# Kernel optimization log

Measured on AMD Instinct MI355X. Metric: run time of the kernel, lower is better.

## Reference

```python
import jax, jax.numpy as jnp
import numpy as np

D = 1024

def setup_inputs() -> dict:
    key = jax.random.key(0)
    ks = jax.random.split(key, 7)
    s = 1.0 / np.sqrt(D)
    return {
        "x": jax.random.normal(ks[0], (4, 2048, D), dtype=jnp.float32),
        "Wq": jax.random.uniform(ks[1], (D, D), jnp.float32, -s, s),
        "bq": jax.random.uniform(ks[2], (D,), jnp.float32, -s, s),
        "Wk": jax.random.uniform(ks[3], (D, D), jnp.float32, -s, s),
        "bk": jax.random.uniform(ks[4], (D,), jnp.float32, -s, s),
        "Wv": jax.random.uniform(ks[5], (D, D), jnp.float32, -s, s),
        "bv": jax.random.uniform(ks[6], (D,), jnp.float32, -s, s),
    }

def reference(x, Wq, bq, Wk, bk, Wv, bv):
    # x: [b, s, d]; Linear layers: y = x @ W^T + b (torch convention)
    q = jnp.einsum('bsd,ed->bse', x, Wq) + bq
    k = jnp.einsum('bsd,ed->bse', x, Wk) + bk
    v = jnp.einsum('bsd,ed->bse', x, Wv) + bv
    # NOTE: original module does NOT scale by 1/sqrt(d)
    scores = jnp.einsum('bqd,bkd->bqk', q, k)  # [b, s, s]
    attn = jax.nn.softmax(scores, axis=-1)
    return jnp.einsum('bqk,bkd->bqd', attn, v)
```

## Files before the change

kernel.cpp:

```cpp
#include <hip/hip_runtime.h>

typedef _Float16 half8 __attribute__((ext_vector_type(8)));
typedef float floatx4 __attribute__((ext_vector_type(4)));

__device__ __forceinline__ void gld_lds16(const void* g, void* l) {
  __builtin_amdgcn_global_load_lds(
      (const __attribute__((address_space(1))) void*)g,
      (__attribute__((address_space(3))) void*)l, 16, 0, 0);
}

#define SB() __builtin_amdgcn_sched_barrier(0)
#define LGKM(n) asm volatile("s_waitcnt lgkmcnt(" #n ")" ::: "memory")
#define VMC(n) asm volatile("s_waitcnt vmcnt(" #n ")" ::: "memory")
#define PRIO1() __builtin_amdgcn_s_setprio(1)
#define PRIO0() __builtin_amdgcn_s_setprio(0)

template <int MODE>
__global__ __launch_bounds__(512, 2) void gemm4(
    const _Float16* __restrict__ Ag, const _Float16* __restrict__ Bg,
    void* __restrict__ Cg, const float* __restrict__ bcat) {
  constexpr int TN   = MODE == 0 ? 192 : (MODE == 1 ? 256 : 128);
  constexpr int STR  = MODE == 0 ? 1024 : (MODE == 1 ? 3072 : 2048);
  constexpr int NK   = (MODE == 2 ? 2048 : 1024) / 64;
  constexpr int NWG  = MODE == 0 ? 512 : 256;
  constexpr int NBC  = TN / 64;
  constexpr int BBUF = TN * 64;
  constexpr int CSTR = MODE == 0 ? 3072 : (MODE == 1 ? 2048 : 1024);

  int g = (int)blockIdx.x;
  g = (g & 7) * (NWG / 8) + (g >> 3);

  int row0, col0;
  const _Float16 *Ap, *Bp;
  _Float16* C16 = nullptr;
  float* C32 = nullptr;
  if constexpr (MODE == 0) {
    const int tm = g >> 4, tn = g & 15;
    row0 = tm * 256; col0 = tn * 192;
    Ap = Ag + (size_t)row0 * 1024;
    Bp = Bg + (size_t)col0 * 1024;
    C16 = (_Float16*)Cg;
  } else if constexpr (MODE == 1) {
    const int z = g >> 6, r = g & 63, tm = r >> 3, tn = r & 7;
    row0 = tm * 256; col0 = tn * 256;
    Ap = Ag + (size_t)z * 6291456 + (size_t)row0 * 3072;
    Bp = Ag + (size_t)z * 6291456 + (size_t)col0 * 3072 + 1024;
    C16 = (_Float16*)Cg + (size_t)z * 4194304;
  } else {
    const int z = g >> 6, r = g & 63, tm = r >> 3, tn = r & 7;
    row0 = tm * 256; col0 = tn * 128;
    Ap = Ag + (size_t)z * 4194304 + (size_t)row0 * 2048;
    Bp = Bg + (size_t)z * 2097152 + (size_t)col0 * 2048;
    C32 = (float*)Cg + (size_t)z * 2097152;
  }

  __shared__ _Float16 lds[32768 + 2 * BBUF];
  const int tid = threadIdx.x, lane = tid & 63, wid = tid >> 6;
  const int wave_m = MODE == 2 ? (wid >> 1) : (wid >> 2);
  const int wave_n = MODE == 2 ? (wid & 1) : (wid & 3);
  const int fr = lane & 15, u = lane >> 4, w7 = lane & 7;
  const int k0e = ((u ^ w7) << 3), k1e = (((4 + u) ^ w7) << 3);
  const int sgl = (((tid & 7) ^ ((tid >> 3) & 7)) << 3);
  const int srow = tid >> 3;

  floatx4 acc[MODE == 2 ? 4 : 8][MODE == 0 ? 3 : 4] = {};
  half8 aF0[8], aF1[8], bF0[4], bF1[4];

  auto stage1 = [&](const _Float16* Gp, int r0c, int kt, int dst) {
    gld_lds16(Gp + (size_t)(r0c + srow) * STR + kt + sgl, &lds[dst + tid * 8]);
  };
  auto ldAq = [&](int bufA, int qm, half8* dst) {
    const int rb = MODE == 2 ? wave_m * 64 : (wave_m * 128 + qm * 64);
#pragma unroll
    for (int mf = 0; mf < 4; ++mf) {
      const int ro = bufA + (rb + mf * 16 + fr) * 64;
      dst[mf * 2 + 0] = *(const half8*)&lds[ro + k0e];
      dst[mf * 2 + 1] = *(const half8*)&lds[ro + k1e];
    }
  };
  auto ldB2 = [&](int bufB, int qh, half8* dst) {
    const int cb = (MODE == 0 ? wave_n * 48 : wave_n * 64) + qh * 32;
#pragma unroll
    for (int nf = 0; nf < 2; ++nf) {
      const int ro = bufB + (cb + nf * 16 + fr) * 64;
      dst[nf * 2 + 0] = *(const half8*)&lds[ro + k0e];
      dst[nf * 2 + 1] = *(const half8*)&lds[ro + k1e];
    }
  };
  auto ldB1 = [&](int bufB, half8* dst) {
    const int ro = bufB + (wave_n * 48 + 32 + fr) * 64;
    dst[0] = *(const half8*)&lds[ro + k0e];
    dst[1] = *(const half8*)&lds[ro + k1e];
  };
  auto QUADx2 = [&](int am0, half8* aF, int nb, half8* bF) {
#pragma unroll
    for (int mf = 0; mf < 4; ++mf)
#pragma unroll
      for (int nf = 0; nf < 2; ++nf)
#pragma unroll
        for (int kk = 0; kk < 2; ++kk)
          acc[am0 + mf][nb + nf] = __builtin_amdgcn_mfma_f32_16x16x32_f16(
              aF[mf * 2 + kk], bF[nf * 2 + kk], acc[am0 + mf][nb + nf], 0, 0, 0);
  };
  auto QUADx1 = [&](int am0, half8* aF, half8* bF) {
#pragma unroll
    for (int mf = 0; mf < 4; ++mf)
#pragma unroll
      for (int kk = 0; kk < 2; ++kk)
        acc[am0 + mf][2] = __builtin_amdgcn_mfma_f32_16x16x32_f16(
            aF[mf * 2 + kk], bF[kk], acc[am0 + mf][2], 0, 0, 0);
  };

#pragma unroll
  for (int c = 0; c < 4; ++c) stage1(Ap, c * 64, 0, c * 4096);
#pragma unroll
  for (int c = 0; c < NBC; ++c) stage1(Bp, c * 64, 0, 32768 + c * 4096);
#pragma unroll
  for (int c = 0; c < NBC; ++c) stage1(Bp, c * 64, 64, 32768 + BBUF + c * 4096);
  if constexpr (NBC == 4) VMC(4); else if constexpr (NBC == 3) VMC(3); else VMC(2);
  __builtin_amdgcn_s_barrier();

#pragma unroll 1
  for (int t = 0; t < NK; ++t) {
    const int kt = t * 64;
    const int bufA = (t & 1) * 16384, obufA = ((t + 1) & 1) * 16384;
    const int bufB = 32768 + (t & 1) * BBUF;
    ldAq(bufA, 0, aF0); SB();
    ldB2(bufB, 0, bF0); SB();
    if constexpr (MODE == 0) { ldB1(bufB, bF1); } else { ldB2(bufB, 1, bF1); }
    SB();
    if constexpr (MODE != 2) { ldAq(bufA, 1, aF1); SB(); }
    if (t + 1 < NK) {
#pragma unroll
      for (int c = 0; c < 4; ++c) stage1(Ap, c * 64, kt + 64, obufA + c * 4096);
    }
    SB();
    if constexpr (MODE == 2) {
      LGKM(4); SB(); PRIO1(); QUADx2(0, aF0, 0, bF0); PRIO0(); SB();
      LGKM(0); SB();
      __builtin_amdgcn_s_barrier();
      if (t + 2 < NK) {
#pragma unroll
        for (int c = 0; c < 2; ++c) stage1(Bp, c * 64, kt + 128, bufB + c * 4096);
      }
      SB();
      PRIO1(); QUADx2(0, aF0, 2, bF1); PRIO0(); SB();
    } else if constexpr (MODE == 1) {
      LGKM(12); SB(); PRIO1(); QUADx2(0, aF0, 0, bF0); PRIO0(); SB();
      LGKM(8);  SB(); PRIO1(); QUADx2(0, aF0, 2, bF1); PRIO0(); SB();
      LGKM(0);  SB(); PRIO1(); QUADx2(4, aF1, 0, bF0); PRIO0(); SB();
      __builtin_amdgcn_s_barrier();
      if (t + 2 < NK) {
#pragma unroll
        for (int c = 0; c < 4; ++c) stage1(Bp, c * 64, kt + 128, bufB + c * 4096);
      }
      SB();
      PRIO1(); QUADx2(4, aF1, 2, bF1); PRIO0(); SB();
    } else {
      LGKM(10); SB(); PRIO1(); QUADx2(0, aF0, 0, bF0); PRIO0(); SB();
      LGKM(8);  SB(); PRIO1(); QUADx1(0, aF0, bF1); PRIO0(); SB();
      LGKM(0);  SB(); PRIO1(); QUADx2(4, aF1, 0, bF0); PRIO0(); SB();
      __builtin_amdgcn_s_barrier();
      if (t + 2 < NK) {
#pragma unroll
        for (int c = 0; c < 3; ++c) stage1(Bp, c * 64, kt + 128, bufB + c * 4096);
      }
      SB();
      PRIO1(); QUADx1(4, aF1, bF1); PRIO0(); SB();
    }
    if (t + 1 < NK) {
      if (t + 2 < NK) {
        if constexpr (NBC == 4) VMC(4); else if constexpr (NBC == 3) VMC(3); else VMC(2);
      } else VMC(0);
    }
    __builtin_amdgcn_s_barrier();
  }

  const int r0 = row0 + (MODE == 2 ? wave_m * 64 : wave_m * 128) + u * 4;
  const int c0 = col0 + (MODE == 0 ? wave_n * 48 : wave_n * 64) + fr;
  constexpr int NMT = MODE == 2 ? 4 : 8;
  constexpr int NFT = MODE == 0 ? 3 : 4;
#pragma unroll
  for (int m = 0; m < NMT; ++m)
#pragma unroll
    for (int n = 0; n < NFT; ++n) {
      const int col = c0 + n * 16;
      float badd = 0.f;
      if constexpr (MODE == 0) badd = bcat[col];
#pragma unroll
      for (int j = 0; j < 4; ++j) {
        const int row = r0 + m * 16 + j;
        if constexpr (MODE == 2)
          C32[(size_t)row * 1024 + col] = acc[m][n][j];
        else
          C16[(size_t)row * CSTR + col] = (_Float16)(acc[m][n][j] + badd);
      }
    }
}

__global__ void cvt_f32_f16(const float* __restrict__ in, _Float16* __restrict__ out, int n8) {
  int i = blockIdx.x * blockDim.x + threadIdx.x;
  const int stride = gridDim.x * blockDim.x;
  for (; i < n8; i += stride) {
    const float4* p = (const float4*)(in + (size_t)i * 8);
    float4 a = p[0], b = p[1];
    half8 h;
    h[0] = (_Float16)a.x; h[1] = (_Float16)a.y; h[2] = (_Float16)a.z; h[3] = (_Float16)a.w;
    h[4] = (_Float16)b.x; h[5] = (_Float16)b.y; h[6] = (_Float16)b.z; h[7] = (_Float16)b.w;
    *(half8*)(out + (size_t)i * 8) = h;
  }
}

__global__ void cvt3_w(const float* __restrict__ wq, const float* __restrict__ wk,
                       const float* __restrict__ wv, _Float16* __restrict__ out) {
  const float* in = blockIdx.y == 0 ? wq : (blockIdx.y == 1 ? wk : wv);
  _Float16* o = out + (size_t)blockIdx.y * 1048576;
  const int i = blockIdx.x * blockDim.x + threadIdx.x;
  const float4* p = (const float4*)(in + (size_t)i * 8);
  float4 a = p[0], b = p[1];
  half8 h;
  h[0] = (_Float16)a.x; h[1] = (_Float16)a.y; h[2] = (_Float16)a.z; h[3] = (_Float16)a.w;
  h[4] = (_Float16)b.x; h[5] = (_Float16)b.y; h[6] = (_Float16)b.z; h[7] = (_Float16)b.w;
  *(half8*)(o + (size_t)i * 8) = h;
}

__global__ void bias_cat(const float* __restrict__ a, const float* __restrict__ b,
                         const float* __restrict__ c, float* __restrict__ o) {
  const int i = blockIdx.x * 256 + threadIdx.x;
  const float* s = i < 1024 ? a : (i < 2048 ? b : c);
  o[i] = s[i & 1023];
}

__global__ __launch_bounds__(256) void transpose_v(const _Float16* __restrict__ QKV,
                                                   _Float16* __restrict__ Vt) {
  __shared__ _Float16 t[32][36];
  const int b = blockIdx.z;
  const int e0 = blockIdx.x * 32;
  const int s0 = blockIdx.y * 32;
  const int tid = threadIdx.x;
  const int r = tid >> 3;
  const int c4 = (tid & 7) * 4;
  const _Float16* src = QKV + (size_t)(b * 2048 + s0 + r) * 3072 + 2048 + e0 + c4;
#pragma unroll
  for (int j = 0; j < 4; ++j) t[r][c4 + j] = src[j];
  __syncthreads();
  _Float16* dst = Vt + ((size_t)b * 1024 + e0 + r) * 2048 + s0 + c4;
#pragma unroll
  for (int j = 0; j < 4; ++j) dst[j] = t[c4 + j][r];
}

__global__ __launch_bounds__(256) void softmax_rows_f16(_Float16* __restrict__ S) {
  __shared__ float red[4];
  _Float16* s = S + (size_t)blockIdx.x * 2048;
  const int tid = threadIdx.x;
  float v[8];
  {
    half8 h = *(const half8*)(s + tid * 8);
#pragma unroll
    for (int j = 0; j < 8; ++j) v[j] = (float)h[j];
  }
  float m = v[0];
#pragma unroll
  for (int j = 1; j < 8; ++j) m = fmaxf(m, v[j]);
#pragma unroll
  for (int off = 32; off > 0; off >>= 1) m = fmaxf(m, __shfl_xor(m, off));
  if ((tid & 63) == 0) red[tid >> 6] = m;
  __syncthreads();
  m = fmaxf(fmaxf(red[0], red[1]), fmaxf(red[2], red[3]));
  float sum = 0.f;
#pragma unroll
  for (int j = 0; j < 8; ++j) { v[j] = __expf(v[j] - m); sum += v[j]; }
#pragma unroll
  for (int off = 32; off > 0; off >>= 1) sum += __shfl_xor(sum, off);
  __syncthreads();
  if ((tid & 63) == 0) red[tid >> 6] = sum;
  __syncthreads();
  sum = red[0] + red[1] + red[2] + red[3];
  const float inv = 1.0f / sum;
  half8 h;
#pragma unroll
  for (int j = 0; j < 8; ++j) h[j] = (_Float16)(v[j] * inv);
  *(half8*)(s + tid * 8) = h;
}

extern "C" void kernel_launch(void* const* d_in, const int* in_sizes, int n_in,
                              void* d_out, int out_size, void* d_ws, size_t ws_size,
                              hipStream_t stream) {
  (void)in_sizes; (void)n_in; (void)out_size;
  const float* x  = (const float*)d_in[0];
  const float* Wq = (const float*)d_in[1];
  const float* bq = (const float*)d_in[2];
  const float* Wk = (const float*)d_in[3];
  const float* bk = (const float*)d_in[4];
  const float* Wv = (const float*)d_in[5];
  const float* bv = (const float*)d_in[6];
  float* out = (float*)d_out;

  char* ws = (char*)d_ws;
  size_t off = 0;
  auto alloc = [&](size_t bytes) {
    char* p = ws + off;
    off += (bytes + 255) & ~255ull;
    return p;
  };
  _Float16* x16  = (_Float16*)alloc(8192ull * 1024 * 2);
  _Float16* W16  = (_Float16*)alloc(3072ull * 1024 * 2);
  _Float16* QKV  = (_Float16*)alloc(8192ull * 3072 * 2);
  _Float16* Vt   = (_Float16*)alloc(4096ull * 1024 * 4);
  _Float16* Sc   = (_Float16*)alloc(4ull * 2048 * 2048 * 2);
  float*    bcat = (float*)alloc(3072 * 4);
  if (off > ws_size) return;

  cvt_f32_f16<<<2048, 256, 0, stream>>>(x, x16, 8192 * 1024 / 8);
  cvt3_w<<<dim3(512, 3), 256, 0, stream>>>(Wq, Wk, Wv, W16);
  bias_cat<<<12, 256, 0, stream>>>(bq, bk, bv, bcat);

  gemm4<0><<<512, 512, 0, stream>>>(x16, W16, QKV, bcat);
  transpose_v<<<dim3(32, 64, 4), 256, 0, stream>>>(QKV, Vt);

  gemm4<1><<<256, 512, 0, stream>>>(QKV, QKV, Sc, nullptr);
  softmax_rows_f16<<<8192, 256, 0, stream>>>(Sc);
  gemm4<2><<<256, 512, 0, stream>>>(Sc, Vt, out, nullptr);
}
```

Before: 165.3 us.

## Rewrite attention GEMMs with 32x32x16 MFMA and per-GEMM specialized kernels

Replaces the templated 16x16x32 MFMA GEMM with three dedicated kernels that use 32x32x16 MFMA instructions. The QKV projection moves to 128x384 tiles, and staging now loads full A+B tiles into double-buffered LDS with barrier-separated burst phases. Larger MFMA tiles cut LDS fragment reads per flop, at the cost of more barriers per iteration, changed overlap of global loads, and larger accumulator register pressure.

```diff
diff --git a/kernel.cpp b/kernel.cpp
--- a/kernel.cpp
+++ b/kernel.cpp
@@ -1,7 +1,7 @@
 #include <hip/hip_runtime.h>
 
 typedef _Float16 half8 __attribute__((ext_vector_type(8)));
-typedef float floatx4 __attribute__((ext_vector_type(4)));
+typedef float f32x16 __attribute__((ext_vector_type(16)));
 
 __device__ __forceinline__ void gld_lds16(const void* g, void* l) {
   __builtin_amdgcn_global_load_lds(
@@ -10,190 +10,264 @@
 }
 
 #define SB() __builtin_amdgcn_sched_barrier(0)
-#define LGKM(n) asm volatile("s_waitcnt lgkmcnt(" #n ")" ::: "memory")
+#define LGKM0() asm volatile("s_waitcnt lgkmcnt(0)" ::: "memory")
+#define LGKM8() asm volatile("s_waitcnt lgkmcnt(8)" ::: "memory")
 #define VMC(n) asm volatile("s_waitcnt vmcnt(" #n ")" ::: "memory")
+#define BAR() __builtin_amdgcn_s_barrier()
 #define PRIO1() __builtin_amdgcn_s_setprio(1)
 #define PRIO0() __builtin_amdgcn_s_setprio(0)
 
-template <int MODE>
-__global__ __launch_bounds__(512, 2) void gemm4(
-    const _Float16* __restrict__ Ag, const _Float16* __restrict__ Bg,
-    void* __restrict__ Cg, const float* __restrict__ bcat) {
-  constexpr int TN   = MODE == 0 ? 192 : (MODE == 1 ? 256 : 128);
-  constexpr int STR  = MODE == 0 ? 1024 : (MODE == 1 ? 3072 : 2048);
-  constexpr int NK   = (MODE == 2 ? 2048 : 1024) / 64;
-  constexpr int NWG  = MODE == 0 ? 512 : 256;
-  constexpr int NBC  = TN / 64;
-  constexpr int BBUF = TN * 64;
-  constexpr int CSTR = MODE == 0 ? 3072 : (MODE == 1 ? 2048 : 1024);
-
+
+__global__ __launch_bounds__(512, 2) void gemm32s(const _Float16* __restrict__ QKV,
+                                                  _Float16* __restrict__ Sc) {
   int g = (int)blockIdx.x;
-  g = (g & 7) * (NWG / 8) + (g >> 3);
-
-  int row0, col0;
-  const _Float16 *Ap, *Bp;
-  _Float16* C16 = nullptr;
-  float* C32 = nullptr;
-  if constexpr (MODE == 0) {
-    const int tm = g >> 4, tn = g & 15;
-    row0 = tm * 256; col0 = tn * 192;
-    Ap = Ag + (size_t)row0 * 1024;
-    Bp = Bg + (size_t)col0 * 1024;
-    C16 = (_Float16*)Cg;
-  } else if constexpr (MODE == 1) {
-    const int z = g >> 6, r = g & 63, tm = r >> 3, tn = r & 7;
-    row0 = tm * 256; col0 = tn * 256;
-    Ap = Ag + (size_t)z * 6291456 + (size_t)row0 * 3072;
-    Bp = Ag + (size_t)z * 6291456 + (size_t)col0 * 3072 + 1024;
-    C16 = (_Float16*)Cg + (size_t)z * 4194304;
-  } else {
-    const int z = g >> 6, r = g & 63, tm = r >> 3, tn = r & 7;
-    row0 = tm * 256; col0 = tn * 128;
-    Ap = Ag + (size_t)z * 4194304 + (size_t)row0 * 2048;
-    Bp = Bg + (size_t)z * 2097152 + (size_t)col0 * 2048;
-    C32 = (float*)Cg + (size_t)z * 2097152;
-  }
-
-  __shared__ _Float16 lds[32768 + 2 * BBUF];
+  g = (g & 7) * 32 + (g >> 3);
+  const int z = g >> 6, r = g & 63, tm = r >> 3, tn = r & 7;
+  const int row0 = tm * 256, col0 = tn * 256;
+  const _Float16* Ap = QKV + ((size_t)z * 2048 + row0) * 3072;
+  const _Float16* Bp = QKV + ((size_t)z * 2048 + col0) * 3072 + 1024;
+  _Float16* C16 = Sc + (size_t)z * 4194304;
+
+  __shared__ _Float16 lds[65536];
   const int tid = threadIdx.x, lane = tid & 63, wid = tid >> 6;
-  const int wave_m = MODE == 2 ? (wid >> 1) : (wid >> 2);
-  const int wave_n = MODE == 2 ? (wid & 1) : (wid & 3);
-  const int fr = lane & 15, u = lane >> 4, w7 = lane & 7;
-  const int k0e = ((u ^ w7) << 3), k1e = (((4 + u) ^ w7) << 3);
-  const int sgl = (((tid & 7) ^ ((tid >> 3) & 7)) << 3);
+  const int wm = wid >> 2, wn = wid & 3;
+  const int l31 = lane & 31, hi = lane >> 5, r7 = l31 & 7;
   const int srow = tid >> 3;
-
-  floatx4 acc[MODE == 2 ? 4 : 8][MODE == 0 ? 3 : 4] = {};
-  half8 aF0[8], aF1[8], bF0[4], bF1[4];
-
-  auto stage1 = [&](const _Float16* Gp, int r0c, int kt, int dst) {
-    gld_lds16(Gp + (size_t)(r0c + srow) * STR + kt + sgl, &lds[dst + tid * 8]);
-  };
-  auto ldAq = [&](int bufA, int qm, half8* dst) {
-    const int rb = MODE == 2 ? wave_m * 64 : (wave_m * 128 + qm * 64);
-#pragma unroll
-    for (int mf = 0; mf < 4; ++mf) {
-      const int ro = bufA + (rb + mf * 16 + fr) * 64;
-      dst[mf * 2 + 0] = *(const half8*)&lds[ro + k0e];
-      dst[mf * 2 + 1] = *(const half8*)&lds[ro + k1e];
-    }
-  };
-  auto ldB2 = [&](int bufB, int qh, half8* dst) {
-    const int cb = (MODE == 0 ? wave_n * 48 : wave_n * 64) + qh * 32;
-#pragma unroll
-    for (int nf = 0; nf < 2; ++nf) {
-      const int ro = bufB + (cb + nf * 16 + fr) * 64;
-      dst[nf * 2 + 0] = *(const half8*)&lds[ro + k0e];
-      dst[nf * 2 + 1] = *(const half8*)&lds[ro + k1e];
-    }
-  };
-  auto ldB1 = [&](int bufB, half8* dst) {
-    const int ro = bufB + (wave_n * 48 + 32 + fr) * 64;
-    dst[0] = *(const half8*)&lds[ro + k0e];
-    dst[1] = *(const half8*)&lds[ro + k1e];
-  };
-  auto QUADx2 = [&](int am0, half8* aF, int nb, half8* bF) {
-#pragma unroll
-    for (int mf = 0; mf < 4; ++mf)
-#pragma unroll
-      for (int nf = 0; nf < 2; ++nf)
-#pragma unroll
-        for (int kk = 0; kk < 2; ++kk)
-          acc[am0 + mf][nb + nf] = __builtin_amdgcn_mfma_f32_16x16x32_f16(
-              aF[mf * 2 + kk], bF[nf * 2 + kk], acc[am0 + mf][nb + nf], 0, 0, 0);
-  };
-  auto QUADx1 = [&](int am0, half8* aF, half8* bF) {
-#pragma unroll
-    for (int mf = 0; mf < 4; ++mf)
-#pragma unroll
-      for (int kk = 0; kk < 2; ++kk)
-        acc[am0 + mf][2] = __builtin_amdgcn_mfma_f32_16x16x32_f16(
-            aF[mf * 2 + kk], bF[kk], acc[am0 + mf][2], 0, 0, 0);
-  };
-
-#pragma unroll
-  for (int c = 0; c < 4; ++c) stage1(Ap, c * 64, 0, c * 4096);
-#pragma unroll
-  for (int c = 0; c < NBC; ++c) stage1(Bp, c * 64, 0, 32768 + c * 4096);
-#pragma unroll
-  for (int c = 0; c < NBC; ++c) stage1(Bp, c * 64, 64, 32768 + BBUF + c * 4096);
-  if constexpr (NBC == 4) VMC(4); else if constexpr (NBC == 3) VMC(3); else VMC(2);
-  __builtin_amdgcn_s_barrier();
-
+  const int sgl = (((tid & 7) ^ (srow & 7)) << 3);
+
+  f32x16 acc[4][2] = {};
+  half8 aF[8], bF0[4], bF1[4];
+
+  auto stage = [&](const _Float16* Gp, int rowoff, int kt, int dstbase) {
+    gld_lds16(Gp + (size_t)(rowoff + srow) * 3072 + kt + sgl, &lds[dstbase + tid * 8]);
+  };
+  auto stageT = [&](int kt, int par) {
+#pragma unroll
+    for (int h = 0; h < 4; ++h) stage(Ap, h * 64, kt, par * 32768 + h * 4096);
+#pragma unroll
+    for (int h = 0; h < 4; ++h) stage(Bp, h * 64, kt, par * 32768 + 16384 + h * 4096);
+  };
+  auto ldA = [&](int par, int qmh) {
+    const int base = par * 32768 + (wm * 128 + qmh * 64 + l31) * 64;
+#pragma unroll
+    for (int mb = 0; mb < 2; ++mb)
+#pragma unroll
+      for (int ks = 0; ks < 4; ++ks)
+        aF[mb * 4 + ks] = *(const half8*)&lds[base + mb * 2048 + (((ks * 2 + hi) ^ r7) << 3)];
+  };
+  auto ldB = [&](int par, int nb, half8* bF) {
+    const int base = par * 32768 + 16384 + (wn * 64 + nb * 32 + l31) * 64;
+#pragma unroll
+    for (int ks = 0; ks < 4; ++ks)
+      bF[ks] = *(const half8*)&lds[base + (((ks * 2 + hi) ^ r7) << 3)];
+  };
+  auto burst = [&](int qmh, int nb, const half8* bF) {
+#pragma unroll
+    for (int ks = 0; ks < 4; ++ks)
+#pragma unroll
+      for (int ml = 0; ml < 2; ++ml)
+        acc[qmh * 2 + ml][nb] = __builtin_amdgcn_mfma_f32_32x32x16_f16(
+            aF[ml * 4 + ks], bF[ks], acc[qmh * 2 + ml][nb], 0, 0, 0);
+  };
+
+  stageT(0, 0);
+  stageT(64, 1);
+  VMC(8); BAR();
+  constexpr int NK = 16;
 #pragma unroll 1
   for (int t = 0; t < NK; ++t) {
-    const int kt = t * 64;
-    const int bufA = (t & 1) * 16384, obufA = ((t + 1) & 1) * 16384;
-    const int bufB = 32768 + (t & 1) * BBUF;
-    ldAq(bufA, 0, aF0); SB();
-    ldB2(bufB, 0, bF0); SB();
-    if constexpr (MODE == 0) { ldB1(bufB, bF1); } else { ldB2(bufB, 1, bF1); }
-    SB();
-    if constexpr (MODE != 2) { ldAq(bufA, 1, aF1); SB(); }
-    if (t + 1 < NK) {
-#pragma unroll
-      for (int c = 0; c < 4; ++c) stage1(Ap, c * 64, kt + 64, obufA + c * 4096);
+    const int par = t & 1;
+    ldA(par, 0); SB(); ldB(par, 0, bF0); SB(); LGKM8();
+    BAR(); LGKM0(); SB(); PRIO1(); burst(0, 0, bF0); PRIO0(); SB(); BAR();
+    ldB(par, 1, bF1); SB();
+    BAR(); LGKM0(); SB(); PRIO1(); burst(0, 1, bF1); PRIO0(); SB(); BAR();
+    ldA(par, 1); SB();
+    BAR(); LGKM0(); SB(); PRIO1(); burst(1, 0, bF0); PRIO0(); SB(); BAR();
+    if (t + 2 < NK) stageT(t * 64 + 128, par);
+    SB(); PRIO1(); burst(1, 1, bF1); PRIO0(); SB();
+    if (t + 2 < NK) { VMC(8); } else if (t + 1 < NK) { VMC(0); }
+    BAR();
+  }
+
+  const int cb = col0 + wn * 64 + l31;
+#pragma unroll
+  for (int mb = 0; mb < 4; ++mb)
+#pragma unroll
+    for (int nb = 0; nb < 2; ++nb) {
+      const int col = cb + nb * 32;
+#pragma unroll
+      for (int j = 0; j < 16; ++j) {
+        const int row = row0 + wm * 128 + mb * 32 + (j & 3) + ((j >> 2) << 3) + hi * 4;
+        C16[(size_t)row * 2048 + col] = (_Float16)acc[mb][nb][j];
+      }
     }
-    SB();
-    if constexpr (MODE == 2) {
-      LGKM(4); SB(); PRIO1(); QUADx2(0, aF0, 0, bF0); PRIO0(); SB();
-      LGKM(0); SB();
-      __builtin_amdgcn_s_barrier();
-      if (t + 2 < NK) {
-#pragma unroll
-        for (int c = 0; c < 2; ++c) stage1(Bp, c * 64, kt + 128, bufB + c * 4096);
+}
+
+__global__ __launch_bounds__(512, 2) void gemm32q(const _Float16* __restrict__ Ag,
+                                                  const _Float16* __restrict__ Bg,
+                                                  _Float16* __restrict__ Cg,
+                                                  const float* __restrict__ bcat) {
+  int g = (int)blockIdx.x;
+  g = (g & 7) * 64 + (g >> 3);
+  const int tm = g >> 3, tn = g & 7;
+  const int row0 = tm * 128, col0 = tn * 384;
+  const _Float16* Ap = Ag + (size_t)row0 * 1024;
+  const _Float16* Bp = Bg + (size_t)col0 * 1024;
+
+  __shared__ _Float16 lds[65536];
+  const int tid = threadIdx.x, lane = tid & 63, wid = tid >> 6;
+  const int wm = wid >> 2, wn = wid & 3;
+  const int l31 = lane & 31, hi = lane >> 5, r7 = l31 & 7;
+  const int srow = tid >> 3;
+  const int sgl = (((tid & 7) ^ (srow & 7)) << 3);
+
+  f32x16 acc[2][3] = {};
+  half8 aF[8], bF[3][4];
+
+  auto stage = [&](const _Float16* Gp, int rowoff, int kt, int dstbase) {
+    gld_lds16(Gp + (size_t)(rowoff + srow) * 1024 + kt + sgl, &lds[dstbase + tid * 8]);
+  };
+  auto stageT = [&](int kt, int par) {
+#pragma unroll
+    for (int h = 0; h < 2; ++h) stage(Ap, h * 64, kt, par * 32768 + h * 4096);
+#pragma unroll
+    for (int h = 0; h < 6; ++h) stage(Bp, h * 64, kt, par * 32768 + 8192 + h * 4096);
+  };
+  auto ldA = [&](int par) {
+    const int base = par * 32768 + (wm * 64 + l31) * 64;
+#pragma unroll
+    for (int mb = 0; mb < 2; ++mb)
+#pragma unroll
+      for (int ks = 0; ks < 4; ++ks)
+        aF[mb * 4 + ks] = *(const half8*)&lds[base + mb * 2048 + (((ks * 2 + hi) ^ r7) << 3)];
+  };
+  auto ldB = [&](int par, int nb) {
+    const int base = par * 32768 + 8192 + (wn * 96 + nb * 32 + l31) * 64;
+#pragma unroll
+    for (int ks = 0; ks < 4; ++ks)
+      bF[nb][ks] = *(const half8*)&lds[base + (((ks * 2 + hi) ^ r7) << 3)];
+  };
+  auto burst = [&](int nb) {
+#pragma unroll
+    for (int ks = 0; ks < 4; ++ks)
+#pragma unroll
+      for (int mb = 0; mb < 2; ++mb)
+        acc[mb][nb] = __builtin_amdgcn_mfma_f32_32x32x16_f16(
+            aF[mb * 4 + ks], bF[nb][ks], acc[mb][nb], 0, 0, 0);
+  };
+
+  stageT(0, 0);
+  VMC(0); BAR();
+  constexpr int NK = 16;
+#pragma unroll 1
+  for (int t = 0; t < NK; ++t) {
+    const int par = t & 1;
+    ldA(par); SB(); ldB(par, 0); SB();
+    if (t + 1 < NK) stageT(t * 64 + 64, par ^ 1);
+    SB(); LGKM8();
+    BAR(); LGKM0(); SB(); PRIO1(); burst(0); PRIO0(); SB(); BAR();
+    ldB(par, 1); SB();
+    BAR(); LGKM0(); SB(); PRIO1(); burst(1); PRIO0(); SB(); BAR();
+    ldB(par, 2); SB();
+    BAR(); LGKM0(); SB(); PRIO1(); burst(2); PRIO0(); SB();
+    if (t + 1 < NK) VMC(0);
+    BAR();
+  }
+
+  const int cb = col0 + wn * 96 + l31;
+#pragma unroll
+  for (int mb = 0; mb < 2; ++mb)
+#pragma unroll
+    for (int nb = 0; nb < 3; ++nb) {
+      const int col = cb + nb * 32;
+      const float badd = bcat[col];
+#pragma unroll
+      for (int j = 0; j < 16; ++j) {
+        const int row = row0 + wm * 64 + mb * 32 + (j & 3) + ((j >> 2) << 3) + hi * 4;
+        Cg[(size_t)row * 3072 + col] = (_Float16)(acc[mb][nb][j] + badd);
       }
-      SB();
-      PRIO1(); QUADx2(0, aF0, 2, bF1); PRIO0(); SB();
-    } else if constexpr (MODE == 1) {
-      LGKM(12); SB(); PRIO1(); QUADx2(0, aF0, 0, bF0); PRIO0(); SB();
-      LGKM(8);  SB(); PRIO1(); QUADx2(0, aF0, 2, bF1); PRIO0(); SB();
-      LGKM(0);  SB(); PRIO1(); QUADx2(4, aF1, 0, bF0); PRIO0(); SB();
-      __builtin_amdgcn_s_barrier();
-      if (t + 2 < NK) {
-#pragma unroll
-        for (int c = 0; c < 4; ++c) stage1(Bp, c * 64, kt + 128, bufB + c * 4096);
-      }
-      SB();
-      PRIO1(); QUADx2(4, aF1, 2, bF1); PRIO0(); SB();
-    } else {
-      LGKM(10); SB(); PRIO1(); QUADx2(0, aF0, 0, bF0); PRIO0(); SB();
-      LGKM(8);  SB(); PRIO1(); QUADx1(0, aF0, bF1); PRIO0(); SB();
-      LGKM(0);  SB(); PRIO1(); QUADx2(4, aF1, 0, bF0); PRIO0(); SB();
-      __builtin_amdgcn_s_barrier();
-      if (t + 2 < NK) {
-#pragma unroll
-        for (int c = 0; c < 3; ++c) stage1(Bp, c * 64, kt + 128, bufB + c * 4096);
-      }
-      SB();
-      PRIO1(); QUADx1(4, aF1, bF1); PRIO0(); SB();
     }
-    if (t + 1 < NK) {
-      if (t + 2 < NK) {
-        if constexpr (NBC == 4) VMC(4); else if constexpr (NBC == 3) VMC(3); else VMC(2);
-      } else VMC(0);
-    }
-    __builtin_amdgcn_s_barrier();
-  }
-
-  const int r0 = row0 + (MODE == 2 ? wave_m * 64 : wave_m * 128) + u * 4;
-  const int c0 = col0 + (MODE == 0 ? wave_n * 48 : wave_n * 64) + fr;
-  constexpr int NMT = MODE == 2 ? 4 : 8;
-  constexpr int NFT = MODE == 0 ? 3 : 4;
-#pragma unroll
-  for (int m = 0; m < NMT; ++m)
-#pragma unroll
-    for (int n = 0; n < NFT; ++n) {
-      const int col = c0 + n * 16;
-      float badd = 0.f;
-      if constexpr (MODE == 0) badd = bcat[col];
-#pragma unroll
-      for (int j = 0; j < 4; ++j) {
-        const int row = r0 + m * 16 + j;
-        if constexpr (MODE == 2)
-          C32[(size_t)row * 1024 + col] = acc[m][n][j];
-        else
-          C16[(size_t)row * CSTR + col] = (_Float16)(acc[m][n][j] + badd);
+}
+
+__global__ __launch_bounds__(512, 2) void gemm32p(const _Float16* __restrict__ Scp,
+                                                  const _Float16* __restrict__ Vt,
+                                                  float* __restrict__ Out) {
+  int g = (int)blockIdx.x;
+  g = (g & 7) * 32 + (g >> 3);
+  const int z = g >> 6, r = g & 63, tm = r >> 3, tn = r & 7;
+  const int row0 = tm * 256, col0 = tn * 128;
+  const _Float16* Ap = Scp + (size_t)z * 4194304 + (size_t)row0 * 2048;
+  const _Float16* Bp = Vt + (size_t)z * 2097152 + (size_t)col0 * 2048;
+  float* C32 = Out + (size_t)z * 2097152;
+
+  __shared__ _Float16 lds[49152];
+  const int tid = threadIdx.x, lane = tid & 63, wid = tid >> 6;
+  const int wm = wid >> 1, wn = wid & 1;
+  const int l31 = lane & 31, hi = lane >> 5, r7 = l31 & 7;
+  const int srow = tid >> 3;
+  const int sgl = (((tid & 7) ^ (srow & 7)) << 3);
+
+  f32x16 acc[2][2] = {};
+  half8 aF[8], bF0[4], bF1[4];
+
+  auto stage = [&](const _Float16* Gp, int rowoff, int kt, int dstbase) {
+    gld_lds16(Gp + (size_t)(rowoff + srow) * 2048 + kt + sgl, &lds[dstbase + tid * 8]);
+  };
+  auto stageT = [&](int kt, int par) {
+#pragma unroll
+    for (int h = 0; h < 4; ++h) stage(Ap, h * 64, kt, par * 24576 + h * 4096);
+#pragma unroll
+    for (int h = 0; h < 2; ++h) stage(Bp, h * 64, kt, par * 24576 + 16384 + h * 4096);
+  };
+  auto ldA = [&](int par) {
+    const int base = par * 24576 + (wm * 64 + l31) * 64;
+#pragma unroll
+    for (int mb = 0; mb < 2; ++mb)
+#pragma unroll
+      for (int ks = 0; ks < 4; ++ks)
+        aF[mb * 4 + ks] = *(const half8*)&lds[base + mb * 2048 + (((ks * 2 + hi) ^ r7) << 3)];
+  };
+  auto ldB = [&](int par, int nb, half8* bF) {
+    const int base = par * 24576 + 16384 + (wn * 64 + nb * 32 + l31) * 64;
+#pragma unroll
+    for (int ks = 0; ks < 4; ++ks)
+      bF[ks] = *(const half8*)&lds[base + (((ks * 2 + hi) ^ r7) << 3)];
+  };
+  auto burst = [&](int nb, const half8* bF) {
+#pragma unroll
+    for (int ks = 0; ks < 4; ++ks)
+#pragma unroll
+      for (int mb = 0; mb < 2; ++mb)
+        acc[mb][nb] = __builtin_amdgcn_mfma_f32_32x32x16_f16(
+            aF[mb * 4 + ks], bF[ks], acc[mb][nb], 0, 0, 0);
+  };
+
+  stageT(0, 0);
+  VMC(0); BAR();
+  constexpr int NK = 32;
+#pragma unroll 1
+  for (int t = 0; t < NK; ++t) {
+    const int par = t & 1;
+    ldA(par); SB(); ldB(par, 0, bF0); SB();
+    if (t + 1 < NK) stageT(t * 64 + 64, par ^ 1);
+    SB(); LGKM8();
+    BAR(); LGKM0(); SB(); PRIO1(); burst(0, bF0); PRIO0(); SB(); BAR();
+    ldB(par, 1, bF1); SB();
+    BAR(); LGKM0(); SB(); PRIO1(); burst(1, bF1); PRIO0(); SB();
+    if (t + 1 < NK) VMC(0);
+    BAR();
+  }
+
+  const int cb = col0 + wn * 64 + l31;
+#pragma unroll
+  for (int mb = 0; mb < 2; ++mb)
+#pragma unroll
+    for (int nb = 0; nb < 2; ++nb) {
+      const int col = cb + nb * 32;
+#pragma unroll
+      for (int j = 0; j < 16; ++j) {
+        const int row = row0 + wm * 64 + mb * 32 + (j & 3) + ((j >> 2) << 3) + hi * 4;
+        C32[(size_t)row * 1024 + col] = acc[mb][nb][j];
       }
     }
 }
@@ -315,10 +389,10 @@
   cvt3_w<<<dim3(512, 3), 256, 0, stream>>>(Wq, Wk, Wv, W16);
   bias_cat<<<12, 256, 0, stream>>>(bq, bk, bv, bcat);
 
-  gemm4<0><<<512, 512, 0, stream>>>(x16, W16, QKV, bcat);
+  gemm32q<<<512, 512, 0, stream>>>(x16, W16, QKV, bcat);
   transpose_v<<<dim3(32, 64, 4), 256, 0, stream>>>(QKV, Vt);
 
-  gemm4<1><<<256, 512, 0, stream>>>(QKV, QKV, Sc, nullptr);
+  gemm32s<<<256, 512, 0, stream>>>(QKV, Sc);
   softmax_rows_f16<<<8192, 256, 0, stream>>>(Sc);
-  gemm4<2><<<256, 512, 0, stream>>>(Sc, Vt, out, nullptr);
-}
+  gemm32p<<<256, 512, 0, stream>>>(Sc, Vt, out);
+}
```

Measured after the change: 183.9 us. +11.3%, slower.

## Simplify GEMM pipeline to uniform double-buffered A/B staging with new wave layouts

Applied to the files above, without the earlier changes.

Replaces the staggered pipeline, where B was prefetched two steps ahead and A one step ahead with a mid-iteration barrier, with a plain double buffer. A and B for the next K step are issued together at the top of each iteration, followed by a single vmcnt(0) wait and one barrier per iteration. It also changes the wave tiling for the QKV and PV GEMMs from a 2x4 and 4x2 layout to 4x2 waves with 4 M fragments each. The aim is fewer barriers and simpler scheduling. The cost is that global loads have only one iteration of compute to hide behind, and a full vmcnt(0) drain every step.

```diff
diff --git a/kernel.cpp b/kernel.cpp
--- a/kernel.cpp
+++ b/kernel.cpp
@@ -11,20 +11,25 @@
 
 #define SB() __builtin_amdgcn_sched_barrier(0)
 #define LGKM(n) asm volatile("s_waitcnt lgkmcnt(" #n ")" ::: "memory")
-#define VMC(n) asm volatile("s_waitcnt vmcnt(" #n ")" ::: "memory")
+#define VMC0() asm volatile("s_waitcnt vmcnt(0)" ::: "memory")
+#define BAR() __builtin_amdgcn_s_barrier()
 #define PRIO1() __builtin_amdgcn_s_setprio(1)
 #define PRIO0() __builtin_amdgcn_s_setprio(0)
 
 template <int MODE>
-__global__ __launch_bounds__(512, 2) void gemm4(
+__global__ __launch_bounds__(512, 2) void gemmr(
     const _Float16* __restrict__ Ag, const _Float16* __restrict__ Bg,
     void* __restrict__ Cg, const float* __restrict__ bcat) {
   constexpr int TN   = MODE == 0 ? 192 : (MODE == 1 ? 256 : 128);
-  constexpr int STR  = MODE == 0 ? 1024 : (MODE == 1 ? 3072 : 2048);
-  constexpr int NK   = (MODE == 2 ? 2048 : 1024) / 64;
+  constexpr int KS   = MODE == 0 ? 1024 : (MODE == 1 ? 3072 : 2048);
+  constexpr int NK   = MODE == 2 ? 32 : 16;
   constexpr int NWG  = MODE == 0 ? 512 : 256;
-  constexpr int NBC  = TN / 64;
-  constexpr int BBUF = TN * 64;
+  constexpr int WN   = MODE == 1 ? 4 : 2;
+  constexpr int NMF  = MODE == 1 ? 8 : 4;
+  constexpr int NNF  = TN / 16 / WN;
+  constexpr int ASL  = 16384;
+  constexpr int BSL  = TN * 64;
+  constexpr int NSB  = TN / 64;
   constexpr int CSTR = MODE == 0 ? 3072 : (MODE == 1 ? 2048 : 1024);
 
   int g = (int)blockIdx.x;
@@ -54,146 +59,102 @@
     C32 = (float*)Cg + (size_t)z * 2097152;
   }
 
-  __shared__ _Float16 lds[32768 + 2 * BBUF];
+  __shared__ _Float16 lds[2 * ASL + 2 * BSL];
   const int tid = threadIdx.x, lane = tid & 63, wid = tid >> 6;
-  const int wave_m = MODE == 2 ? (wid >> 1) : (wid >> 2);
-  const int wave_n = MODE == 2 ? (wid & 1) : (wid & 3);
+  const int wm = MODE == 1 ? (wid >> 2) : (wid >> 1);
+  const int wn = MODE == 1 ? (wid & 3) : (wid & 1);
+  const int wrow = wm * (NMF * 16);
+  const int wcol = wn * (NNF * 16);
   const int fr = lane & 15, u = lane >> 4, w7 = lane & 7;
   const int k0e = ((u ^ w7) << 3), k1e = (((4 + u) ^ w7) << 3);
-  const int sgl = (((tid & 7) ^ ((tid >> 3) & 7)) << 3);
   const int srow = tid >> 3;
-
-  floatx4 acc[MODE == 2 ? 4 : 8][MODE == 0 ? 3 : 4] = {};
-  half8 aF0[8], aF1[8], bF0[4], bF1[4];
-
-  auto stage1 = [&](const _Float16* Gp, int r0c, int kt, int dst) {
-    gld_lds16(Gp + (size_t)(r0c + srow) * STR + kt + sgl, &lds[dst + tid * 8]);
-  };
-  auto ldAq = [&](int bufA, int qm, half8* dst) {
-    const int rb = MODE == 2 ? wave_m * 64 : (wave_m * 128 + qm * 64);
+  const int sgl = (((tid & 7) ^ (srow & 7)) << 3);
+
+  floatx4 acc[NMF][NNF] = {};
+  half8 aF[NMF * 2], bF[NNF * 2];
+
+  auto stage1 = [&](const _Float16* Gp, int rowoff, int kt, int dst) {
+    gld_lds16(Gp + (size_t)(rowoff + srow) * KS + kt + sgl, &lds[dst + tid * 8]);
+  };
+  auto stageT = [&](int kt, int p) {
+#pragma unroll
+    for (int c = 0; c < 4; ++c) stage1(Ap, c * 64, kt, p * ASL + c * 4096);
+#pragma unroll
+    for (int c = 0; c < NSB; ++c)
+      stage1(Bp, c * 64, kt, 2 * ASL + p * BSL + c * 4096);
+  };
+  auto ldA4 = [&](int p, int mf0) {
 #pragma unroll
     for (int mf = 0; mf < 4; ++mf) {
-      const int ro = bufA + (rb + mf * 16 + fr) * 64;
-      dst[mf * 2 + 0] = *(const half8*)&lds[ro + k0e];
-      dst[mf * 2 + 1] = *(const half8*)&lds[ro + k1e];
-    }
-  };
-  auto ldB2 = [&](int bufB, int qh, half8* dst) {
-    const int cb = (MODE == 0 ? wave_n * 48 : wave_n * 64) + qh * 32;
+      const int ro = p * ASL + (wrow + (mf0 + mf) * 16 + fr) * 64;
+      aF[(mf0 + mf) * 2 + 0] = *(const half8*)&lds[ro + k0e];
+      aF[(mf0 + mf) * 2 + 1] = *(const half8*)&lds[ro + k1e];
+    }
+  };
+  auto ldB2 = [&](int p, int nf0) {
 #pragma unroll
     for (int nf = 0; nf < 2; ++nf) {
-      const int ro = bufB + (cb + nf * 16 + fr) * 64;
-      dst[nf * 2 + 0] = *(const half8*)&lds[ro + k0e];
-      dst[nf * 2 + 1] = *(const half8*)&lds[ro + k1e];
-    }
-  };
-  auto ldB1 = [&](int bufB, half8* dst) {
-    const int ro = bufB + (wave_n * 48 + 32 + fr) * 64;
-    dst[0] = *(const half8*)&lds[ro + k0e];
-    dst[1] = *(const half8*)&lds[ro + k1e];
-  };
-  auto QUADx2 = [&](int am0, half8* aF, int nb, half8* bF) {
+      const int ro = 2 * ASL + p * BSL + (wcol + (nf0 + nf) * 16 + fr) * 64;
+      bF[(nf0 + nf) * 2 + 0] = *(const half8*)&lds[ro + k0e];
+      bF[(nf0 + nf) * 2 + 1] = *(const half8*)&lds[ro + k1e];
+    }
+  };
+  auto burst = [&](int mf0, int nf0) {
 #pragma unroll
     for (int mf = 0; mf < 4; ++mf)
 #pragma unroll
       for (int nf = 0; nf < 2; ++nf)
 #pragma unroll
         for (int kk = 0; kk < 2; ++kk)
-          acc[am0 + mf][nb + nf] = __builtin_amdgcn_mfma_f32_16x16x32_f16(
-              aF[mf * 2 + kk], bF[nf * 2 + kk], acc[am0 + mf][nb + nf], 0, 0, 0);
-  };
-  auto QUADx1 = [&](int am0, half8* aF, half8* bF) {
-#pragma unroll
-    for (int mf = 0; mf < 4; ++mf)
-#pragma unroll
-      for (int kk = 0; kk < 2; ++kk)
-        acc[am0 + mf][2] = __builtin_amdgcn_mfma_f32_16x16x32_f16(
-            aF[mf * 2 + kk], bF[kk], acc[am0 + mf][2], 0, 0, 0);
-  };
-
-#pragma unroll
-  for (int c = 0; c < 4; ++c) stage1(Ap, c * 64, 0, c * 4096);
-#pragma unroll
-  for (int c = 0; c < NBC; ++c) stage1(Bp, c * 64, 0, 32768 + c * 4096);
-#pragma unroll
-  for (int c = 0; c < NBC; ++c) stage1(Bp, c * 64, 64, 32768 + BBUF + c * 4096);
-  if constexpr (NBC == 4) VMC(4); else if constexpr (NBC == 3) VMC(3); else VMC(2);
-  __builtin_amdgcn_s_barrier();
+          acc[mf0 + mf][nf0 + nf] = __builtin_amdgcn_mfma_f32_16x16x32_f16(
+              aF[(mf0 + mf) * 2 + kk], bF[(nf0 + nf) * 2 + kk],
+              acc[mf0 + mf][nf0 + nf], 0, 0, 0);
+  };
+
+  stageT(0, 0);
+  VMC0();
+  BAR();
 
 #pragma unroll 1
   for (int t = 0; t < NK; ++t) {
-    const int kt = t * 64;
-    const int bufA = (t & 1) * 16384, obufA = ((t + 1) & 1) * 16384;
-    const int bufB = 32768 + (t & 1) * BBUF;
-    ldAq(bufA, 0, aF0); SB();
-    ldB2(bufB, 0, bF0); SB();
-    if constexpr (MODE == 0) { ldB1(bufB, bF1); } else { ldB2(bufB, 1, bF1); }
+    const int p = t & 1;
+    if (t + 1 < NK) stageT(t * 64 + 64, p ^ 1);
     SB();
-    if constexpr (MODE != 2) { ldAq(bufA, 1, aF1); SB(); }
-    if (t + 1 < NK) {
-#pragma unroll
-      for (int c = 0; c < 4; ++c) stage1(Ap, c * 64, kt + 64, obufA + c * 4096);
-    }
-    SB();
-    if constexpr (MODE == 2) {
-      LGKM(4); SB(); PRIO1(); QUADx2(0, aF0, 0, bF0); PRIO0(); SB();
-      LGKM(0); SB();
-      __builtin_amdgcn_s_barrier();
-      if (t + 2 < NK) {
-#pragma unroll
-        for (int c = 0; c < 2; ++c) stage1(Bp, c * 64, kt + 128, bufB + c * 4096);
-      }
-      SB();
-      PRIO1(); QUADx2(0, aF0, 2, bF1); PRIO0(); SB();
-    } else if constexpr (MODE == 1) {
-      LGKM(12); SB(); PRIO1(); QUADx2(0, aF0, 0, bF0); PRIO0(); SB();
-      LGKM(8);  SB(); PRIO1(); QUADx2(0, aF0, 2, bF1); PRIO0(); SB();
-      LGKM(0);  SB(); PRIO1(); QUADx2(4, aF1, 0, bF0); PRIO0(); SB();
-      __builtin_amdgcn_s_barrier();
-      if (t + 2 < NK) {
-#pragma unroll
-        for (int c = 0; c < 4; ++c) stage1(Bp, c * 64, kt + 128, bufB + c * 4096);
-      }
-      SB();
-      PRIO1(); QUADx2(4, aF1, 2, bF1); PRIO0(); SB();
+    if constexpr (MODE == 1) {
+      ldA4(p, 0); SB(); ldB2(p, 0); SB(); ldB2(p, 2); SB(); ldA4(p, 4); SB();
+      LGKM(12); SB(); PRIO1(); burst(0, 0); PRIO0(); SB();
+      LGKM(8);  SB(); PRIO1(); burst(0, 2); PRIO0(); SB();
+      LGKM(0);  SB(); PRIO1(); burst(4, 0); burst(4, 2); PRIO0(); SB();
+    } else if constexpr (MODE == 0) {
+      ldA4(p, 0); SB(); ldB2(p, 0); SB(); ldB2(p, 2); SB(); ldB2(p, 4); SB();
+      LGKM(8); SB(); PRIO1(); burst(0, 0); PRIO0(); SB();
+      LGKM(4); SB(); PRIO1(); burst(0, 2); PRIO0(); SB();
+      LGKM(0); SB(); PRIO1(); burst(0, 4); PRIO0(); SB();
     } else {
-      LGKM(10); SB(); PRIO1(); QUADx2(0, aF0, 0, bF0); PRIO0(); SB();
-      LGKM(8);  SB(); PRIO1(); QUADx1(0, aF0, bF1); PRIO0(); SB();
-      LGKM(0);  SB(); PRIO1(); QUADx2(4, aF1, 0, bF0); PRIO0(); SB();
-      __builtin_amdgcn_s_barrier();
-      if (t + 2 < NK) {
-#pragma unroll
-        for (int c = 0; c < 3; ++c) stage1(Bp, c * 64, kt + 128, bufB + c * 4096);
-      }
-      SB();
-      PRIO1(); QUADx1(4, aF1, bF1); PRIO0(); SB();
-    }
-    if (t + 1 < NK) {
-      if (t + 2 < NK) {
-        if constexpr (NBC == 4) VMC(4); else if constexpr (NBC == 3) VMC(3); else VMC(2);
-      } else VMC(0);
-    }
-    __builtin_amdgcn_s_barrier();
-  }
-
-  const int r0 = row0 + (MODE == 2 ? wave_m * 64 : wave_m * 128) + u * 4;
-  const int c0 = col0 + (MODE == 0 ? wave_n * 48 : wave_n * 64) + fr;
-  constexpr int NMT = MODE == 2 ? 4 : 8;
-  constexpr int NFT = MODE == 0 ? 3 : 4;
-#pragma unroll
-  for (int m = 0; m < NMT; ++m)
-#pragma unroll
-    for (int n = 0; n < NFT; ++n) {
-      const int col = c0 + n * 16;
+      ldA4(p, 0); SB(); ldB2(p, 0); SB(); ldB2(p, 2); SB();
+      LGKM(4); SB(); PRIO1(); burst(0, 0); PRIO0(); SB();
+      LGKM(0); SB(); PRIO1(); burst(0, 2); PRIO0(); SB();
+    }
+    if (t + 1 < NK) VMC0();
+    BAR();
+  }
+
+  const int r0 = row0 + wrow + u * 4;
+  const int c0 = col0 + wcol + fr;
+#pragma unroll
+  for (int mf = 0; mf < NMF; ++mf)
+#pragma unroll
+    for (int nf = 0; nf < NNF; ++nf) {
+      const int col = c0 + nf * 16;
       float badd = 0.f;
       if constexpr (MODE == 0) badd = bcat[col];
 #pragma unroll
       for (int j = 0; j < 4; ++j) {
-        const int row = r0 + m * 16 + j;
+        const int row = r0 + mf * 16 + j;
         if constexpr (MODE == 2)
-          C32[(size_t)row * 1024 + col] = acc[m][n][j];
+          C32[(size_t)row * CSTR + col] = acc[mf][nf][j];
         else
-          C16[(size_t)row * CSTR + col] = (_Float16)(acc[m][n][j] + badd);
+          C16[(size_t)row * CSTR + col] = (_Float16)(acc[mf][nf][j] + badd);
       }
     }
 }
@@ -315,10 +276,10 @@
   cvt3_w<<<dim3(512, 3), 256, 0, stream>>>(Wq, Wk, Wv, W16);
   bias_cat<<<12, 256, 0, stream>>>(bq, bk, bv, bcat);
 
-  gemm4<0><<<512, 512, 0, stream>>>(x16, W16, QKV, bcat);
+  gemmr<0><<<512, 512, 0, stream>>>(x16, W16, QKV, bcat);
   transpose_v<<<dim3(32, 64, 4), 256, 0, stream>>>(QKV, Vt);
 
-  gemm4<1><<<256, 512, 0, stream>>>(QKV, QKV, Sc, nullptr);
+  gemmr<1><<<256, 512, 0, stream>>>(QKV, QKV, Sc, nullptr);
   softmax_rows_f16<<<8192, 256, 0, stream>>>(Sc);
-  gemm4<2><<<256, 512, 0, stream>>>(Sc, Vt, out, nullptr);
-}
+  gemmr<2><<<256, 512, 0, stream>>>(Sc, Vt, out, nullptr);
+}
```

Measured after the change: 163.0 us. No clear change (-1.4%).
